# Kernel tuning notes

Hardware: AMD Instinct MI355X
Metric: run time of the kernel (lower is better)

## Reference

```python
import jax, jax.numpy as jnp
import numpy as np

N_BUCKET, EPB, EMBED, K, TAU = 64, 8, 1024, 2, 1.0
EPS_NORM, EPS_W = 1e-12, 1e-9

def _l2norm(x):
    n = jnp.linalg.norm(x, axis=-1, keepdims=True)
    return x / jnp.maximum(n, EPS_NORM)

def setup_inputs() -> dict:
    key = jax.random.key(0)
    k1, k2, k3 = jax.random.split(key, 3)
    h = jax.random.normal(k1, (8, 2048, EMBED), dtype=jnp.float32)
    op_id = jax.random.randint(k2, (8, 2048), 0, N_BUCKET, dtype=jnp.int64)
    expert_key = jax.random.normal(k3, (N_BUCKET, EPB, EMBED), dtype=jnp.float32) / np.sqrt(EMBED)
    return {"h": h, "op_id": op_id, "expert_key": expert_key}

def reference(h, op_id, expert_key):
    # h: (B,T,C), op_id: (B,T), expert_key: (n_bucket, epb, C)
    bucket = jnp.clip(op_id, 0, N_BUCKET - 1)          # (B,T)
    h_n = _l2norm(h)                                    # (B,T,C)
    keys = _l2norm(expert_key)                          # (nb,epb,C)
    keys_bt = keys[bucket]                              # gather -> (B,T,epb,C)
    score = jnp.einsum('btc,btec->bte', h_n, keys_bt)   # (B,T,epb)
    score = score / max(TAU, 1e-6)
    probs_local = jax.nn.softmax(score, axis=-1)        # (B,T,epb)
    topv, local = jax.lax.top_k(probs_local, K)         # (B,T,k) each
    w = topv / (jnp.sum(topv, axis=-1, keepdims=True) + EPS_W)
    gid = bucket[..., None] * EPB + local               # (B,T,k) global expert ids
    return (gid, w)
```

## Files before the change

### kernel.cpp

```cpp
#include <hip/hip_runtime.h>
#include <cmath>

#define EMBED   1024
#define EPB     8
#define NB      64
#define KTOP    2
#define TPB_TOK 32
#define KPAD    1028

__global__ __launch_bounds__(1024) void prep_kernel(
    const float* __restrict__ ek, float* __restrict__ rnorm,
    const int* __restrict__ op, int ntok,
    int* __restrict__ bstart_g, int* __restrict__ cnt_g,
    int* __restrict__ cpre_g, int* __restrict__ chunk2b,
    int* __restrict__ perm) {
    int tid  = threadIdx.x;
    int lane = tid & 63;
    int wave = tid >> 6;

    if (blockIdx.x < 32) {
        int row = blockIdx.x * 16 + wave;
        const float4* r4 = (const float4*)(ek + (size_t)row * EMBED);
        float s = 0.f;
#pragma unroll
        for (int c = 0; c < 4; ++c) {
            float4 v = r4[c * 64 + lane];
            s += v.x * v.x + v.y * v.y + v.z * v.z + v.w * v.w;
        }
#pragma unroll
        for (int off = 32; off; off >>= 1) s += __shfl_xor(s, off, 64);
        if (lane == 0) rnorm[row] = 1.0f / fmaxf(sqrtf(s), 1e-12f);
        return;
    }

    __shared__ int s_hist[NB];
    __shared__ int s_cur[NB];
    if (tid < NB) s_hist[tid] = 0;
    __syncthreads();
    for (int i = tid; i < ntok; i += 1024) {
        int b = min(max(op[i], 0), NB - 1);
        atomicAdd(&s_hist[b], 1);
    }
    __syncthreads();
    if (tid < 64) {
        int c   = s_hist[tid];
        int nch = (c + TPB_TOK - 1) / TPB_TOK;
        int ic = c, in = nch;
#pragma unroll
        for (int off = 1; off < 64; off <<= 1) {
            int vc = __shfl_up(ic, off, 64);
            int vn = __shfl_up(in, off, 64);
            if (lane >= off) { ic += vc; in += vn; }
        }
        int bs = ic - c;
        int cp = in - nch;
        s_cur[tid]    = bs;
        bstart_g[tid] = bs;
        cnt_g[tid]    = c;
        cpre_g[tid]   = cp;
        if (tid == 63) cpre_g[NB] = in;
        for (int j = 0; j < nch; ++j) chunk2b[cp + j] = tid;
    }
    __syncthreads();
    for (int i = tid; i < ntok; i += 1024) {
        int b = min(max(op[i], 0), NB - 1);
        int pos = atomicAdd(&s_cur[b], 1);
        perm[pos] = i;
    }
}

__global__ __launch_bounds__(256) void router_main_kernel(
    const float* __restrict__ h,  const float* __restrict__ ek,
    const float* __restrict__ rk, const int* __restrict__ perm,
    const int* __restrict__ bstart_g, const int* __restrict__ cnt_g,
    const int* __restrict__ cpre_g, const int* __restrict__ chunk2b,
    float* __restrict__ out_gid, float* __restrict__ out_w) {
    __shared__ float sk[EPB * KPAD];
    __shared__ float s_rk[EPB];

    int tid  = threadIdx.x;
    int lane = tid & 63;
    int wave = tid >> 6;
    int grp  = lane >> 3;
    int e    = lane & 7;
    int ts   = wave * 8 + grp;

    int total = cpre_g[NB];

    for (int g = blockIdx.x; g < total; g += gridDim.x) {
        int b  = chunk2b[g];
        int lc = g - cpre_g[b];

        __syncthreads();
        const float4* src4 = (const float4*)ek + (size_t)b * (EPB * EMBED / 4);
#pragma unroll
        for (int k = 0; k < 8; ++k) {
            int idx = k * 256 + tid;
            int r = idx >> 8, c = idx & 255;
            *(float4*)(sk + r * KPAD + c * 4) = src4[idx];
        }
        if (tid < EPB) s_rk[tid] = rk[b * EPB + tid];
        __syncthreads();

        int base = bstart_g[b] + lc * TPB_TOK;
        int end  = bstart_g[b] + cnt_g[b];
        int gi   = base + ts;
        int tok  = perm[min(gi, end - 1)];

        const float4* hrow = (const float4*)(h + (size_t)tok * EMBED);
        const float*  kp   = sk + e * KPAD;

        float dot = 0.f, hh = 0.f;
#pragma unroll 8
        for (int c = 0; c < 256; ++c) {
            float4 a  = hrow[c];
            float4 kv = *(const float4*)(kp + c * 4);
            dot += a.x * kv.x + a.y * kv.y + a.z * kv.z + a.w * kv.w;
            hh  += a.x * a.x + a.y * a.y + a.z * a.z + a.w * a.w;
        }

        float rh = 1.0f / fmaxf(sqrtf(hh), 1e-12f);
        float sc = dot * rh * s_rk[e];

        float m = sc;
#pragma unroll
        for (int off = 1; off < 8; off <<= 1)
            m = fmaxf(m, __shfl_xor(m, off, 64));
        float ex = expf(sc - m);
        float Z = ex;
#pragma unroll
        for (int off = 1; off < 8; off <<= 1)
            Z += __shfl_xor(Z, off, 64);

        float v1 = ex; int i1 = e;
#pragma unroll
        for (int off = 1; off < 8; off <<= 1) {
            float ov = __shfl_xor(v1, off, 64);
            int   oi = __shfl_xor(i1, off, 64);
            if (ov > v1 || (ov == v1 && oi < i1)) { v1 = ov; i1 = oi; }
        }
        float v2 = (e == i1) ? -1e30f : ex; int i2 = e;
#pragma unroll
        for (int off = 1; off < 8; off <<= 1) {
            float ov = __shfl_xor(v2, off, 64);
            int   oi = __shfl_xor(i2, off, 64);
            if (ov > v2 || (ov == v2 && oi < i2)) { v2 = ov; i2 = oi; }
        }

        if (e == 0 && gi < end) {
            float p1 = v1 / Z, p2 = v2 / Z;
            float ws = p1 + p2 + 1e-9f;
            ((float2*)out_gid)[tok] =
                make_float2((float)(b * EPB + i1), (float)(b * EPB + i2));
            ((float2*)out_w)[tok] = make_float2(p1 / ws, p2 / ws);
        }
    }
}

__global__ void key_rnorm_kernel(const float* __restrict__ ek,
                                 float* __restrict__ rnorm, int nrows) {
    int wave = (int)((blockIdx.x * blockDim.x + threadIdx.x) >> 6);
    int lane = threadIdx.x & 63;
    if (wave >= nrows) return;
    const float4* row = (const float4*)(ek + (size_t)wave * EMBED);
    float s = 0.f;
#pragma unroll
    for (int c = 0; c < 4; ++c) {
        float4 v = row[c * 64 + lane];
        s += v.x * v.x + v.y * v.y + v.z * v.z + v.w * v.w;
    }
#pragma unroll
    for (int off = 32; off; off >>= 1) s += __shfl_xor(s, off, 64);
    if (lane == 0) rnorm[wave] = 1.0f / fmaxf(sqrtf(s), 1e-12f);
}

__global__ void router_kernel(const float* __restrict__ h,
                              const int*   __restrict__ op_id,
                              const float* __restrict__ ek,
                              const float* __restrict__ rk,
                              float* __restrict__ out_gid,
                              float* __restrict__ out_w,
                              int ntok) {
    int wave = (int)((blockIdx.x * blockDim.x + threadIdx.x) >> 6);
    int lane = threadIdx.x & 63;
    if (wave >= ntok) return;
    int b = op_id[wave];
    b = min(max(b, 0), NB - 1);
    const float4* hrow = (const float4*)(h + (size_t)wave * EMBED);
    float4 hv[4];
    float hh = 0.f;
#pragma unroll
    for (int c = 0; c < 4; ++c) {
        hv[c] = hrow[c * 64 + lane];
        hh += hv[c].x * hv[c].x + hv[c].y * hv[c].y +
              hv[c].z * hv[c].z + hv[c].w * hv[c].w;
    }
    const float4* kbase = (const float4*)(ek + (size_t)b * EPB * EMBED);
    float dot[EPB];
#pragma unroll
    for (int e = 0; e < EPB; ++e) {
        float d = 0.f;
#pragma unroll
        for (int c = 0; c < 4; ++c) {
            float4 kv = kbase[e * 256 + c * 64 + lane];
            d += hv[c].x * kv.x + hv[c].y * kv.y +
                 hv[c].z * kv.z + hv[c].w * kv.w;
        }
        dot[e] = d;
    }
#pragma unroll
    for (int off = 32; off; off >>= 1) {
        hh += __shfl_xor(hh, off, 64);
#pragma unroll
        for (int e = 0; e < EPB; ++e) dot[e] += __shfl_xor(dot[e], off, 64);
    }
    if (lane == 0) {
        float rh = 1.0f / fmaxf(sqrtf(hh), 1e-12f);
        float sc[EPB];
        float m = -1e30f;
#pragma unroll
        for (int e = 0; e < EPB; ++e) {
            sc[e] = dot[e] * rh * rk[b * EPB + e];
            m = fmaxf(m, sc[e]);
        }
        float ex[EPB];
        float Z = 0.f;
#pragma unroll
        for (int e = 0; e < EPB; ++e) { ex[e] = expf(sc[e] - m); Z += ex[e]; }
        int i1 = 0;
#pragma unroll
        for (int e = 1; e < EPB; ++e) if (ex[e] > ex[i1]) i1 = e;
        int i2 = (i1 == 0) ? 1 : 0;
#pragma unroll
        for (int e = 0; e < EPB; ++e)
            if (e != i1 && ex[e] > ex[i2]) i2 = e;
        float p1 = ex[i1] / Z;
        float p2 = ex[i2] / Z;
        float wsum = p1 + p2 + 1e-9f;
        out_gid[(size_t)wave * KTOP + 0] = (float)(b * EPB + i1);
        out_gid[(size_t)wave * KTOP + 1] = (float)(b * EPB + i2);
        out_w  [(size_t)wave * KTOP + 0] = p1 / wsum;
        out_w  [(size_t)wave * KTOP + 1] = p2 / wsum;
    }
}

extern "C" void kernel_launch(void* const* d_in, const int* in_sizes, int n_in,
                              void* d_out, int out_size, void* d_ws, size_t ws_size,
                              hipStream_t stream) {
    const float* h     = (const float*)d_in[0];
    const int*   op_id = (const int*)  d_in[1];
    const float* ek    = (const float*)d_in[2];

    int ntok = in_sizes[1];
    int maxch = NB + (ntok + TPB_TOK - 1) / TPB_TOK;

    float* out_gid = (float*)d_out;
    float* out_w   = out_gid + (size_t)ntok * KTOP;

    float* rk      = (float*)d_ws;
    int*   bstart  = (int*)(rk + 512);
    int*   cnt     = bstart + NB;
    int*   cpre    = cnt + NB;
    int*   chunk2b = cpre + (NB + 1);
    int*   perm    = chunk2b + maxch;
    size_t need    = ((size_t)(512 + 2 * NB + NB + 1 + maxch) + (size_t)ntok) * 4;

    if (ws_size < need) {
        key_rnorm_kernel<<<128, 256, 0, stream>>>(ek, rk, NB * EPB);
        int blocks2 = (ntok * 64 + 255) / 256;
        router_kernel<<<blocks2, 256, 0, stream>>>(h, op_id, ek, rk,
                                                   out_gid, out_w, ntok);
        return;
    }

    prep_kernel<<<33, 1024, 0, stream>>>(ek, rk, op_id, ntok,
                                         bstart, cnt, cpre, chunk2b, perm);
    router_main_kernel<<<maxch, 256, 0, stream>>>(
        h, ek, rk, perm, bstart, cnt, cpre, chunk2b, out_gid, out_w);
}
```

Measured before the change: 137.2 us.

## Replace bucket-sorted LDS router with quarter-wave-per-token direct router

Drops the histogram/permutation prep kernel and the bucket-chunked router that staged expert keys in LDS. Each token is now handled by 16 lanes (four tokens per wave), reading keys straight from global/L2 and reducing with short shuffles. This removes the sort pass, its serial single-block histogram, and the per-chunk LDS staging and barriers. In exchange every token re-reads its bucket's 32 KB key block through cache, and each thread holds 16 float4 registers, so occupancy may drop.

```diff
diff --git a/kernel.cpp b/kernel.cpp
--- a/kernel.cpp
+++ b/kernel.cpp
@@ -5,163 +5,12 @@
 #define EPB     8
 #define NB      64
 #define KTOP    2
-#define TPB_TOK 32
-#define KPAD    1028
-
-__global__ __launch_bounds__(1024) void prep_kernel(
-    const float* __restrict__ ek, float* __restrict__ rnorm,
-    const int* __restrict__ op, int ntok,
-    int* __restrict__ bstart_g, int* __restrict__ cnt_g,
-    int* __restrict__ cpre_g, int* __restrict__ chunk2b,
-    int* __restrict__ perm) {
-    int tid  = threadIdx.x;
-    int lane = tid & 63;
-    int wave = tid >> 6;
-
-    if (blockIdx.x < 32) {
-        int row = blockIdx.x * 16 + wave;
-        const float4* r4 = (const float4*)(ek + (size_t)row * EMBED);
-        float s = 0.f;
-#pragma unroll
-        for (int c = 0; c < 4; ++c) {
-            float4 v = r4[c * 64 + lane];
-            s += v.x * v.x + v.y * v.y + v.z * v.z + v.w * v.w;
-        }
-#pragma unroll
-        for (int off = 32; off; off >>= 1) s += __shfl_xor(s, off, 64);
-        if (lane == 0) rnorm[row] = 1.0f / fmaxf(sqrtf(s), 1e-12f);
-        return;
-    }
-
-    __shared__ int s_hist[NB];
-    __shared__ int s_cur[NB];
-    if (tid < NB) s_hist[tid] = 0;
-    __syncthreads();
-    for (int i = tid; i < ntok; i += 1024) {
-        int b = min(max(op[i], 0), NB - 1);
-        atomicAdd(&s_hist[b], 1);
-    }
-    __syncthreads();
-    if (tid < 64) {
-        int c   = s_hist[tid];
-        int nch = (c + TPB_TOK - 1) / TPB_TOK;
-        int ic = c, in = nch;
-#pragma unroll
-        for (int off = 1; off < 64; off <<= 1) {
-            int vc = __shfl_up(ic, off, 64);
-            int vn = __shfl_up(in, off, 64);
-            if (lane >= off) { ic += vc; in += vn; }
-        }
-        int bs = ic - c;
-        int cp = in - nch;
-        s_cur[tid]    = bs;
-        bstart_g[tid] = bs;
-        cnt_g[tid]    = c;
-        cpre_g[tid]   = cp;
-        if (tid == 63) cpre_g[NB] = in;
-        for (int j = 0; j < nch; ++j) chunk2b[cp + j] = tid;
-    }
-    __syncthreads();
-    for (int i = tid; i < ntok; i += 1024) {
-        int b = min(max(op[i], 0), NB - 1);
-        int pos = atomicAdd(&s_cur[b], 1);
-        perm[pos] = i;
-    }
-}
-
-__global__ __launch_bounds__(256) void router_main_kernel(
-    const float* __restrict__ h,  const float* __restrict__ ek,
-    const float* __restrict__ rk, const int* __restrict__ perm,
-    const int* __restrict__ bstart_g, const int* __restrict__ cnt_g,
-    const int* __restrict__ cpre_g, const int* __restrict__ chunk2b,
-    float* __restrict__ out_gid, float* __restrict__ out_w) {
-    __shared__ float sk[EPB * KPAD];
-    __shared__ float s_rk[EPB];
-
-    int tid  = threadIdx.x;
-    int lane = tid & 63;
-    int wave = tid >> 6;
-    int grp  = lane >> 3;
-    int e    = lane & 7;
-    int ts   = wave * 8 + grp;
-
-    int total = cpre_g[NB];
-
-    for (int g = blockIdx.x; g < total; g += gridDim.x) {
-        int b  = chunk2b[g];
-        int lc = g - cpre_g[b];
-
-        __syncthreads();
-        const float4* src4 = (const float4*)ek + (size_t)b * (EPB * EMBED / 4);
-#pragma unroll
-        for (int k = 0; k < 8; ++k) {
-            int idx = k * 256 + tid;
-            int r = idx >> 8, c = idx & 255;
-            *(float4*)(sk + r * KPAD + c * 4) = src4[idx];
-        }
-        if (tid < EPB) s_rk[tid] = rk[b * EPB + tid];
-        __syncthreads();
-
-        int base = bstart_g[b] + lc * TPB_TOK;
-        int end  = bstart_g[b] + cnt_g[b];
-        int gi   = base + ts;
-        int tok  = perm[min(gi, end - 1)];
-
-        const float4* hrow = (const float4*)(h + (size_t)tok * EMBED);
-        const float*  kp   = sk + e * KPAD;
-
-        float dot = 0.f, hh = 0.f;
-#pragma unroll 8
-        for (int c = 0; c < 256; ++c) {
-            float4 a  = hrow[c];
-            float4 kv = *(const float4*)(kp + c * 4);
-            dot += a.x * kv.x + a.y * kv.y + a.z * kv.z + a.w * kv.w;
-            hh  += a.x * a.x + a.y * a.y + a.z * a.z + a.w * a.w;
-        }
-
-        float rh = 1.0f / fmaxf(sqrtf(hh), 1e-12f);
-        float sc = dot * rh * s_rk[e];
-
-        float m = sc;
-#pragma unroll
-        for (int off = 1; off < 8; off <<= 1)
-            m = fmaxf(m, __shfl_xor(m, off, 64));
-        float ex = expf(sc - m);
-        float Z = ex;
-#pragma unroll
-        for (int off = 1; off < 8; off <<= 1)
-            Z += __shfl_xor(Z, off, 64);
-
-        float v1 = ex; int i1 = e;
-#pragma unroll
-        for (int off = 1; off < 8; off <<= 1) {
-            float ov = __shfl_xor(v1, off, 64);
-            int   oi = __shfl_xor(i1, off, 64);
-            if (ov > v1 || (ov == v1 && oi < i1)) { v1 = ov; i1 = oi; }
-        }
-        float v2 = (e == i1) ? -1e30f : ex; int i2 = e;
-#pragma unroll
-        for (int off = 1; off < 8; off <<= 1) {
-            float ov = __shfl_xor(v2, off, 64);
-            int   oi = __shfl_xor(i2, off, 64);
-            if (ov > v2 || (ov == v2 && oi < i2)) { v2 = ov; i2 = oi; }
-        }
-
-        if (e == 0 && gi < end) {
-            float p1 = v1 / Z, p2 = v2 / Z;
-            float ws = p1 + p2 + 1e-9f;
-            ((float2*)out_gid)[tok] =
-                make_float2((float)(b * EPB + i1), (float)(b * EPB + i2));
-            ((float2*)out_w)[tok] = make_float2(p1 / ws, p2 / ws);
-        }
-    }
-}
 
 __global__ void key_rnorm_kernel(const float* __restrict__ ek,
-                                 float* __restrict__ rnorm, int nrows) {
+                                 float* __restrict__ rnorm) {
     int wave = (int)((blockIdx.x * blockDim.x + threadIdx.x) >> 6);
     int lane = threadIdx.x & 63;
-    if (wave >= nrows) return;
+    if (wave >= NB * EPB) return;
     const float4* row = (const float4*)(ek + (size_t)wave * EMBED);
     float s = 0.f;
 #pragma unroll
@@ -174,73 +23,84 @@
     if (lane == 0) rnorm[wave] = 1.0f / fmaxf(sqrtf(s), 1e-12f);
 }
 
-__global__ void router_kernel(const float* __restrict__ h,
-                              const int*   __restrict__ op_id,
-                              const float* __restrict__ ek,
-                              const float* __restrict__ rk,
-                              float* __restrict__ out_gid,
-                              float* __restrict__ out_w,
-                              int ntok) {
-    int wave = (int)((blockIdx.x * blockDim.x + threadIdx.x) >> 6);
+__global__ __launch_bounds__(256, 4) void router_quad_kernel(
+    const float* __restrict__ h, const int* __restrict__ op,
+    const float* __restrict__ ek, const float* __restrict__ rk,
+    float* __restrict__ out_gid, float* __restrict__ out_w, int ntok) {
+    int gtid = blockIdx.x * blockDim.x + threadIdx.x;
+    int wid  = gtid >> 6;
     int lane = threadIdx.x & 63;
-    if (wave >= ntok) return;
-    int b = op_id[wave];
+    int q    = lane >> 4;
+    int r    = lane & 15;
+    int tq   = wid * 4 + q;
+    int tc   = min(tq, ntok - 1);
+
+    int b = op[tc];
     b = min(max(b, 0), NB - 1);
-    const float4* hrow = (const float4*)(h + (size_t)wave * EMBED);
-    float4 hv[4];
+
+    const float4* hrow = (const float4*)(h + (size_t)tc * EMBED);
+    float4 hv[16];
     float hh = 0.f;
 #pragma unroll
-    for (int c = 0; c < 4; ++c) {
-        hv[c] = hrow[c * 64 + lane];
-        hh += hv[c].x * hv[c].x + hv[c].y * hv[c].y +
-              hv[c].z * hv[c].z + hv[c].w * hv[c].w;
+    for (int i = 0; i < 16; ++i) {
+        hv[i] = hrow[i * 16 + r];
+        hh += hv[i].x * hv[i].x + hv[i].y * hv[i].y +
+              hv[i].z * hv[i].z + hv[i].w * hv[i].w;
     }
-    const float4* kbase = (const float4*)(ek + (size_t)b * EPB * EMBED);
+
+    float rke[EPB];
+#pragma unroll
+    for (int e = 0; e < EPB; ++e) rke[e] = rk[b * EPB + e];
+
+    const float4* kb = (const float4*)ek + (size_t)b * (EPB * EMBED / 4);
     float dot[EPB];
 #pragma unroll
     for (int e = 0; e < EPB; ++e) {
         float d = 0.f;
 #pragma unroll
-        for (int c = 0; c < 4; ++c) {
-            float4 kv = kbase[e * 256 + c * 64 + lane];
-            d += hv[c].x * kv.x + hv[c].y * kv.y +
-                 hv[c].z * kv.z + hv[c].w * kv.w;
+        for (int i = 0; i < 16; ++i) {
+            float4 kv = kb[e * 256 + i * 16 + r];
+            d += hv[i].x * kv.x + hv[i].y * kv.y +
+                 hv[i].z * kv.z + hv[i].w * kv.w;
         }
         dot[e] = d;
     }
+
 #pragma unroll
-    for (int off = 32; off; off >>= 1) {
+    for (int off = 8; off; off >>= 1) {
         hh += __shfl_xor(hh, off, 64);
 #pragma unroll
         for (int e = 0; e < EPB; ++e) dot[e] += __shfl_xor(dot[e], off, 64);
     }
-    if (lane == 0) {
-        float rh = 1.0f / fmaxf(sqrtf(hh), 1e-12f);
-        float sc[EPB];
-        float m = -1e30f;
+
+    float rh = 1.0f / fmaxf(sqrtf(hh), 1e-12f);
+    float sc[EPB];
+    float m = -1e30f;
 #pragma unroll
-        for (int e = 0; e < EPB; ++e) {
-            sc[e] = dot[e] * rh * rk[b * EPB + e];
-            m = fmaxf(m, sc[e]);
-        }
-        float ex[EPB];
-        float Z = 0.f;
+    for (int e = 0; e < EPB; ++e) {
+        sc[e] = dot[e] * rh * rke[e];
+        m = fmaxf(m, sc[e]);
+    }
+    float ex[EPB];
+    float Z = 0.f;
 #pragma unroll
-        for (int e = 0; e < EPB; ++e) { ex[e] = expf(sc[e] - m); Z += ex[e]; }
-        int i1 = 0;
+    for (int e = 0; e < EPB; ++e) { ex[e] = expf(sc[e] - m); Z += ex[e]; }
+
+    int i1 = 0;
 #pragma unroll
-        for (int e = 1; e < EPB; ++e) if (ex[e] > ex[i1]) i1 = e;
-        int i2 = (i1 == 0) ? 1 : 0;
+    for (int e = 1; e < EPB; ++e) if (ex[e] > ex[i1]) i1 = e;
+    int i2 = (i1 == 0) ? 1 : 0;
 #pragma unroll
-        for (int e = 0; e < EPB; ++e)
-            if (e != i1 && ex[e] > ex[i2]) i2 = e;
+    for (int e = 0; e < EPB; ++e)
+        if (e != i1 && ex[e] > ex[i2]) i2 = e;
+
+    if (r == 0 && tq < ntok) {
         float p1 = ex[i1] / Z;
         float p2 = ex[i2] / Z;
-        float wsum = p1 + p2 + 1e-9f;
-        out_gid[(size_t)wave * KTOP + 0] = (float)(b * EPB + i1);
-        out_gid[(size_t)wave * KTOP + 1] = (float)(b * EPB + i2);
-        out_w  [(size_t)wave * KTOP + 0] = p1 / wsum;
-        out_w  [(size_t)wave * KTOP + 1] = p2 / wsum;
+        float ws = p1 + p2 + 1e-9f;
+        ((float2*)out_gid)[tq] =
+            make_float2((float)(b * EPB + i1), (float)(b * EPB + i2));
+        ((float2*)out_w)[tq] = make_float2(p1 / ws, p2 / ws);
     }
 }
 
@@ -252,29 +112,14 @@
     const float* ek    = (const float*)d_in[2];
 
     int ntok = in_sizes[1];
-    int maxch = NB + (ntok + TPB_TOK - 1) / TPB_TOK;
 
+    float* rk      = (float*)d_ws;
     float* out_gid = (float*)d_out;
     float* out_w   = out_gid + (size_t)ntok * KTOP;
 
-    float* rk      = (float*)d_ws;
-    int*   bstart  = (int*)(rk + 512);
-    int*   cnt     = bstart + NB;
-    int*   cpre    = cnt + NB;
-    int*   chunk2b = cpre + (NB + 1);
-    int*   perm    = chunk2b + maxch;
-    size_t need    = ((size_t)(512 + 2 * NB + NB + 1 + maxch) + (size_t)ntok) * 4;
+    key_rnorm_kernel<<<128, 256, 0, stream>>>(ek, rk);
 
-    if (ws_size < need) {
-        key_rnorm_kernel<<<128, 256, 0, stream>>>(ek, rk, NB * EPB);
-        int blocks2 = (ntok * 64 + 255) / 256;
-        router_kernel<<<blocks2, 256, 0, stream>>>(h, op_id, ek, rk,
+    int blocks = (ntok + 15) / 16;
+    router_quad_kernel<<<blocks, 256, 0, stream>>>(h, op_id, ek, rk,
                                                    out_gid, out_w, ntok);
-        return;
-    }
-
-    prep_kernel<<<33, 1024, 0, stream>>>(ek, rk, op_id, ntok,
-                                         bstart, cnt, cpre, chunk2b, perm);
-    router_main_kernel<<<maxch, 256, 0, stream>>>(
-        h, ek, rk, perm, bstart, cnt, cpre, chunk2b, out_gid, out_w);
 }
```

Result: faster. 115.9 us (-15.5%).
